# Kernel tuning notes

Hardware: AMD Instinct MI355X
Metric: run time of the kernel (lower is better)

The kernel has to match this reference:

```python
import jax, jax.numpy as jnp
import numpy as np

EMB = 768
BLOCK = 64
K = EMB // BLOCK  # 12


def setup_inputs() -> dict:
    key = jax.random.key(0)
    ks = jax.random.split(key, 8)
    n, c, d, h, E, M, P = 4, 1024, 768, 12, 32, 4, 256
    seq = jax.random.normal(ks[0], (n, c, d), dtype=jnp.float32)
    attn = jax.random.uniform(ks[1], (n, h, c, c), dtype=jnp.float32)
    attn = attn / attn.sum(-1, keepdims=True)  # attention-like rows
    mention_pos = jax.random.randint(ks[2], (n, E, M), 0, c)
    hts = jax.random.randint(ks[3], (n, P, 2), 0, E)
    W_head = jax.random.normal(ks[4], (2 * d, EMB), dtype=jnp.float32) / np.sqrt(2 * d)
    W_tail = jax.random.normal(ks[5], (2 * d, EMB), dtype=jnp.float32) / np.sqrt(2 * d)
    W_bil = jax.random.normal(ks[6], (EMB * BLOCK, 97), dtype=jnp.float32) / np.sqrt(EMB * BLOCK)
    return {
        "sequence_output": seq,
        "attention": attn,
        "mention_pos": mention_pos,
        "hts": hts,
        "W_head": W_head,
        "b_head": jnp.zeros((EMB,), jnp.float32),
        "W_tail": W_tail,
        "b_tail": jnp.zeros((EMB,), jnp.float32),
        "W_bil": W_bil,
        "b_bil": jnp.zeros((97,), jnp.float32),
    }


def reference(sequence_output, attention, mention_pos, hts,
              W_head, b_head, W_tail, b_tail, W_bil, b_bil):
    n, c, d = sequence_output.shape
    h = attention.shape[1]
    P = hts.shape[1]

    bidx = jnp.arange(n)[:, None, None]
    # gather mention token embeddings: [n, E, M, d]
    m_emb = sequence_output[bidx, mention_pos]
    # entity embedding = logsumexp over mentions (single-mention case is identical)
    ent_emb = jax.nn.logsumexp(m_emb, axis=2)                      # [n, E, d]

    # per-mention attention rows: attention[i, :, pos, :] -> [n, E, M, h, c]
    att_t = jnp.transpose(attention, (0, 2, 1, 3))                 # [n, c, h, c]
    m_att = att_t[bidx, mention_pos]                               # [n, E, M, h, c]
    ent_att = m_att.mean(axis=2)                                   # [n, E, h, c]

    pidx = jnp.arange(n)[:, None]
    hs = ent_emb[pidx, hts[..., 0]]                                # [n, P, d]
    ts = ent_emb[pidx, hts[..., 1]]
    h_att = ent_att[pidx, hts[..., 0]]                             # [n, P, h, c]
    t_att = ent_att[pidx, hts[..., 1]]

    ht_att = (h_att * t_att).mean(axis=2)                          # [n, P, c]
    ht_att = ht_att / (ht_att.sum(-1, keepdims=True) + 1e-30)
    # relation context: contract('ld,rl->rd') per doc
    rs = jnp.einsum('ncd,npc->npd', sequence_output, ht_att)       # [n, P, d]

    R = n * P
    hs2 = jnp.tanh(jnp.concatenate([hs, rs], -1).reshape(R, 2 * d) @ W_head + b_head)
    ts2 = jnp.tanh(jnp.concatenate([ts, rs], -1).reshape(R, 2 * d) @ W_tail + b_tail)

    b1 = hs2.reshape(R, K, BLOCK)
    b2 = ts2.reshape(R, K, BLOCK)
    bl = (b1[:, :, :, None] * b2[:, :, None, :]).reshape(R, EMB * BLOCK)
    logits = bl @ W_bil + b_bil                                    # [R, 97]
    return logits
```

## Files before the change

kernel.cpp:

```cpp
#include <hip/hip_runtime.h>
#include <hip/hip_bf16.h>
#include <math.h>

#define ND 4
#define CL 1024
#define DD 768
#define HH 12
#define EE 32
#define MMEN 4
#define PP 256
#define EMBD 768
#define KBL 12
#define OUTD 97
#define RTOT (ND*PP)
#define NSPLIT 48

typedef unsigned short u16;
typedef __attribute__((ext_vector_type(8))) short short8;
typedef __attribute__((ext_vector_type(8))) _Float16 half8;
typedef __attribute__((ext_vector_type(4))) float f32x4;

static __device__ inline float bf16u_to_f(unsigned v){
  union { unsigned u; float f; } c; c.u = v << 16; return c.f;
}
static __device__ inline unsigned f_to_bf16u(float f){
  union { float f; unsigned u; } c; c.f = f;
  return (c.u + 0x7fffu + ((c.u >> 16) & 1u)) >> 16;
}
static __device__ inline u16 f_to_f16u(float f){
  _Float16 h = (_Float16)f;
  union { _Float16 h; u16 u; } c; c.h = h; return c.u;
}

#define GLOAD_LDS16(gp, lp) __builtin_amdgcn_global_load_lds( \
    (const __attribute__((address_space(1))) unsigned*)(gp), \
    (__attribute__((address_space(3))) unsigned*)(lp), 16, 0, 0)

__global__ __launch_bounds__(256) void k_ent_emb(const float* __restrict__ seq,
    const int* __restrict__ mpos, u16* __restrict__ ent_emb_bf,
    float* __restrict__ S)
{
  int idx = blockIdx.x*256 + threadIdx.x;
  if (idx >= ND*EE*DD) return;
  if (idx < RTOT) S[idx] = 0.f;
  int dd = idx % DD;
  int e  = (idx / DD) % EE;
  int i  = idx / (DD*EE);
  const int* mp = mpos + (i*EE + e)*MMEN;
  float v[MMEN];
  float mx = -1e30f;
  #pragma unroll
  for (int m=0;m<MMEN;m++){
    v[m] = seq[(i*CL + mp[m])*DD + dd];
    mx = fmaxf(mx, v[m]);
  }
  float s = 0.f;
  #pragma unroll
  for (int m=0;m<MMEN;m++) s += expf(v[m]-mx);
  ent_emb_bf[idx] = (u16)f_to_bf16u(mx + logf(s));
}

__global__ __launch_bounds__(256) void k_ent_att(const float* __restrict__ attn,
    const int* __restrict__ mpos, u16* __restrict__ ent_att_bf)
{
  int idx = blockIdx.x*256 + threadIdx.x;
  if (idx >= ND*EE*HH*(CL/8)) return;
  int j8   = idx % (CL/8);
  int head = (idx / (CL/8)) % HH;
  int e    = (idx / (CL/8*HH)) % EE;
  int i    = idx / (CL/8*HH*EE);
  const int* mp = mpos + (i*EE + e)*MMEN;
  float acc[8] = {};
  #pragma unroll
  for (int m=0;m<MMEN;m++){
    const float4* p = (const float4*)(attn +
        ((size_t)(i*HH + head)*CL + mp[m])*CL + j8*8);
    float4 a = p[0], b = p[1];
    acc[0]+=a.x; acc[1]+=a.y; acc[2]+=a.z; acc[3]+=a.w;
    acc[4]+=b.x; acc[5]+=b.y; acc[6]+=b.z; acc[7]+=b.w;
  }
  unsigned o[4];
  #pragma unroll
  for (int q=0;q<4;q++){
    unsigned lo = f_to_bf16u(acc[2*q]   * (1.f/MMEN));
    unsigned hi = f_to_bf16u(acc[2*q+1] * (1.f/MMEN));
    o[q] = lo | (hi<<16);
  }
  ((uint4*)ent_att_bf)[idx] = make_uint4(o[0],o[1],o[2],o[3]);
}

__global__ __launch_bounds__(256) void k_ht_att(const u16* __restrict__ ent_att_bf,
    const int* __restrict__ hts, u16* __restrict__ u_ht_bf, float* __restrict__ S)
{
  const int j0  = blockIdx.x*64;
  const int pb  = blockIdx.y*64;
  const int doc = blockIdx.z;
  const int tid = threadIdx.x;
  const int p_local = tid >> 2, quad = tid & 3;
  const int grow = doc*PP + pb + p_local;
  const int he = hts[grow*2+0], te = hts[grow*2+1];
  const u16* ha = ent_att_bf + ((size_t)(doc*EE + he)*HH)*CL;
  const u16* ta = ent_att_bf + ((size_t)(doc*EE + te)*HH)*CL;
  const int jj = j0 + quad*16;

  float acc[16] = {};
  #pragma unroll
  for (int h=0; h<HH; h++){
    const uint4* pa = (const uint4*)(ha + h*CL + jj);
    const uint4* pb4 = (const uint4*)(ta + h*CL + jj);
    uint4 a0 = pa[0], a1 = pa[1];
    uint4 b0 = pb4[0], b1 = pb4[1];
    unsigned ua[8] = {a0.x,a0.y,a0.z,a0.w,a1.x,a1.y,a1.z,a1.w};
    unsigned ub[8] = {b0.x,b0.y,b0.z,b0.w,b1.x,b1.y,b1.z,b1.w};
    #pragma unroll
    for (int q=0;q<8;q++){
      acc[2*q]   += bf16u_to_f(ua[q]&0xffffu) * bf16u_to_f(ub[q]&0xffffu);
      acc[2*q+1] += bf16u_to_f(ua[q]>>16)     * bf16u_to_f(ub[q]>>16);
    }
  }
  float sum = 0.f;
  unsigned o[8];
  #pragma unroll
  for (int q=0;q<8;q++){
    float v0 = acc[2*q]   * (1.f/HH);
    float v1 = acc[2*q+1] * (1.f/HH);
    sum += v0 + v1;
    o[q] = f_to_bf16u(v0) | (f_to_bf16u(v1)<<16);
  }
  uint4* dst = (uint4*)(u_ht_bf + (size_t)grow*CL + jj);
  dst[0] = make_uint4(o[0],o[1],o[2],o[3]);
  dst[1] = make_uint4(o[4],o[5],o[6],o[7]);
  sum += __shfl_xor(sum, 1, 64);
  sum += __shfl_xor(sum, 2, 64);
  if (quad == 0) atomicAdd(&S[grow], sum);
}

__global__ __launch_bounds__(256) void k_transpose_bf(const float* __restrict__ src,
    u16* __restrict__ dst, int R, int C)
{
  size_t boff = (size_t)blockIdx.z * R * C;
  src += boff; dst += boff;
  __shared__ float t[32][33];
  int tx = threadIdx.x & 31, ty = threadIdx.x >> 5;
  int c0 = blockIdx.x*32, r0 = blockIdx.y*32;
  #pragma unroll
  for (int q=0;q<4;q++)
    t[ty+8*q][tx] = src[(size_t)(r0+ty+8*q)*C + c0+tx];
  __syncthreads();
  #pragma unroll
  for (int q=0;q<4;q++)
    dst[(size_t)(c0+ty+8*q)*R + r0+tx] = (u16)f_to_bf16u(t[tx][ty+8*q]);
}

__global__ __launch_bounds__(256) void k_transpose_bf_w(
    const float* __restrict__ srcA, u16* __restrict__ dstA,
    const float* __restrict__ srcB, u16* __restrict__ dstB, int R, int C)
{
  const float* src = blockIdx.z ? srcB : srcA;
  u16* dst         = blockIdx.z ? dstB : dstA;
  __shared__ float t[32][33];
  int tx = threadIdx.x & 31, ty = threadIdx.x >> 5;
  int c0 = blockIdx.x*32, r0 = blockIdx.y*32;
  #pragma unroll
  for (int q=0;q<4;q++)
    t[ty+8*q][tx] = src[(size_t)(r0+ty+8*q)*C + c0+tx];
  __syncthreads();
  #pragma unroll
  for (int q=0;q<4;q++)
    dst[(size_t)(c0+ty+8*q)*R + r0+tx] = (u16)f_to_bf16u(t[tx][ty+8*q]);
}

__global__ __launch_bounds__(256) void k_gemm_rs_mfma(
    const u16* __restrict__ u_ht_bf, const u16* __restrict__ seq_t_bf,
    const float* __restrict__ S, u16* __restrict__ rs_bf)
{
  const int rt = blockIdx.x, ct = blockIdx.y, doc = blockIdx.z;
  const u16* A  = u_ht_bf + (size_t)doc*PP*CL;
  const u16* Bt = seq_t_bf + (size_t)doc*DD*CL;
  const int row0 = rt*128, col0 = ct*64;
  __shared__ __align__(16) u16 As[128*64];
  __shared__ __align__(16) u16 Bs[64*64];
  const int tid = threadIdx.x, lane = tid & 63, wave = tid >> 6;
  const int m = lane & 15, j8 = lane >> 4;
  const int srow8 = lane >> 3, sc8 = lane & 7;
  f32x4 acc[2][4];
  #pragma unroll
  for (int a=0;a<2;a++)
    #pragma unroll
    for (int b=0;b<4;b++) acc[a][b] = (f32x4){0.f,0.f,0.f,0.f};

  for (int k0 = 0; k0 < CL; k0 += 64){
    __syncthreads();
    #pragma unroll
    for (int ii=0; ii<4; ii++){
      int row = ii*32 + wave*8 + srow8;
      int gc = sc8 ^ (row & 7);
      const u16* gp = A + (size_t)(row0+row)*CL + k0 + gc*8;
      GLOAD_LDS16(gp, &As[(ii*32 + wave*8)*64]);
    }
    #pragma unroll
    for (int ii=0; ii<2; ii++){
      int row = ii*32 + wave*8 + srow8;
      int gc = sc8 ^ (row & 7);
      const u16* gp = Bt + (size_t)(col0+row)*CL + k0 + gc*8;
      GLOAD_LDS16(gp, &Bs[(ii*32 + wave*8)*64]);
    }
    __syncthreads();
    #pragma unroll
    for (int h=0; h<2; h++){
      short8 af[2], bf[4];
      #pragma unroll
      for (int mf=0; mf<2; mf++){
        int r = wave*32 + mf*16 + m;
        int c = (h*4 + j8) ^ (r & 7);
        af[mf] = *(const short8*)&As[r*64 + c*8];
      }
      #pragma unroll
      for (int nt=0; nt<4; nt++){
        int n = nt*16 + m;
        int c = (h*4 + j8) ^ (n & 7);
        bf[nt] = *(const short8*)&Bs[n*64 + c*8];
      }
      #pragma unroll
      for (int mf=0; mf<2; mf++)
        #pragma unroll
        for (int nt=0; nt<4; nt++)
          acc[mf][nt] = __builtin_amdgcn_mfma_f32_16x16x32_bf16(af[mf], bf[nt], acc[mf][nt], 0,0,0);
    }
  }

  #pragma unroll
  for (int mf=0; mf<2; mf++){
    #pragma unroll
    for (int nt=0; nt<4; nt++){
      int colg = col0 + nt*16 + m;
      #pragma unroll
      for (int reg=0; reg<4; reg++){
        int rowg = doc*PP + row0 + wave*32 + mf*16 + j8*4 + reg;
        float sc = 1.f / (S[rowg] + 1e-30f);
        rs_bf[(size_t)rowg*DD + colg] = (u16)f_to_bf16u(acc[mf][nt][reg] * sc);
      }
    }
  }
}

__global__ __launch_bounds__(256) void k_gemm_ht_mfma(
    const u16* __restrict__ ent_emb_bf, const u16* __restrict__ rs_bf,
    const int* __restrict__ hts,
    const u16* __restrict__ Wht, const u16* __restrict__ Wtt,
    const float* __restrict__ b_head, const float* __restrict__ b_tail,
    u16* __restrict__ hs2h, u16* __restrict__ ts2h)
{
  const int rt = blockIdx.x, ct = blockIdx.y, z = blockIdx.z;
  const u16* Bt   = z ? Wtt : Wht;
  const float* bias = z ? b_tail : b_head;
  u16* C          = z ? ts2h : hs2h;
  const int row0 = rt*128, col0 = ct*64;
  __shared__ __align__(16) u16 As[128*64];
  __shared__ __align__(16) u16 Bs[64*64];
  const int tid = threadIdx.x, lane = tid & 63, wave = tid >> 6;
  const int m = lane & 15, j8 = lane >> 4;
  const int srow8 = lane >> 3, sc8 = lane & 7;

  const u16* gEnt[4]; const u16* gRs[4]; int gcA[4];
  #pragma unroll
  for (int ii=0; ii<4; ii++){
    int row  = ii*32 + wave*8 + srow8;
    int grow = row0 + row;
    int ent  = hts[grow*2 + z];
    gEnt[ii] = ent_emb_bf + ((size_t)((grow>>8)*EE + ent))*DD;
    gRs[ii]  = rs_bf + (size_t)grow*DD;
    gcA[ii]  = (sc8 ^ (row & 7)) * 8;
  }

  f32x4 acc[2][4];
  #pragma unroll
  for (int a=0;a<2;a++)
    #pragma unroll
    for (int b=0;b<4;b++) acc[a][b] = (f32x4){0.f,0.f,0.f,0.f};

  for (int k0 = 0; k0 < 1536; k0 += 64){
    __syncthreads();
    #pragma unroll
    for (int ii=0; ii<4; ii++){
      const u16* gp = (k0 < DD) ? (gEnt[ii] + k0 + gcA[ii])
                                : (gRs[ii] + (k0-DD) + gcA[ii]);
      GLOAD_LDS16(gp, &As[(ii*32 + wave*8)*64]);
    }
    #pragma unroll
    for (int ii=0; ii<2; ii++){
      int row = ii*32 + wave*8 + srow8;
      int gc = sc8 ^ (row & 7);
      const u16* gp = Bt + (size_t)(col0+row)*1536 + k0 + gc*8;
      GLOAD_LDS16(gp, &Bs[(ii*32 + wave*8)*64]);
    }
    __syncthreads();
    #pragma unroll
    for (int h=0; h<2; h++){
      short8 af[2], bf[4];
      #pragma unroll
      for (int mf=0; mf<2; mf++){
        int r = wave*32 + mf*16 + m;
        int c = (h*4 + j8) ^ (r & 7);
        af[mf] = *(const short8*)&As[r*64 + c*8];
      }
      #pragma unroll
      for (int nt=0; nt<4; nt++){
        int n = nt*16 + m;
        int c = (h*4 + j8) ^ (n & 7);
        bf[nt] = *(const short8*)&Bs[n*64 + c*8];
      }
      #pragma unroll
      for (int mf=0; mf<2; mf++)
        #pragma unroll
        for (int nt=0; nt<4; nt++)
          acc[mf][nt] = __builtin_amdgcn_mfma_f32_16x16x32_bf16(af[mf], bf[nt], acc[mf][nt], 0,0,0);
    }
  }

  #pragma unroll
  for (int mf=0; mf<2; mf++){
    #pragma unroll
    for (int nt=0; nt<4; nt++){
      int colg = col0 + nt*16 + m;
      float bv = bias[colg];
      #pragma unroll
      for (int reg=0; reg<4; reg++){
        int rowg = row0 + wave*32 + mf*16 + j8*4 + reg;
        C[(size_t)rowg*DD + colg] = f_to_f16u(tanhf(acc[mf][nt][reg] + bv));
      }
    }
  }
}

__global__ __launch_bounds__(256) void k_wt2(const float* __restrict__ W_bil,
    u16* __restrict__ Wt2)
{
  const int cc = blockIdx.x;
  __shared__ u16 lds2[4480];
  int tid = threadIdx.x;
  for (int u=tid; u<4480; u+=256) lds2[u] = 0;
  __syncthreads();
  for (int u=tid; u<112*32; u+=256){
    int kk = u / 112, n = u % 112;
    if (n < OUTD)
      lds2[n*40 + kk] = f_to_f16u(W_bil[(size_t)(cc*32 + kk)*OUTD + n]);
  }
  __syncthreads();
  uint4* dst = (uint4*)(Wt2 + (size_t)cc*4480);
  const uint4* src = (const uint4*)lds2;
  for (int v=tid; v<560; v+=256) dst[v] = src[v];
}

__global__ __launch_bounds__(256) void k_bilinear(
    const u16* __restrict__ hs2h, const u16* __restrict__ ts2h,
    const u16* __restrict__ Wt2, float* __restrict__ pbuf)
{
  const int rt = blockIdx.x;
  const int sp = blockIdx.y;
  const int kb = sp >> 2;
  const int i0 = (sp & 3) * 16;
  const int row0 = rt * 128;

  __shared__ __align__(16) u16 b1s[128][24];
  __shared__ __align__(16) u16 b2s[128][72];
  __shared__ __align__(16) u16 Ws[4480];

  const int tid = threadIdx.x;
  const int lane = tid & 63, wave = tid >> 6;
  const int m = lane & 15, j8 = lane >> 4;

  {
    int r = tid >> 1, half = tid & 1;
    uint4 v = *(const uint4*)&hs2h[(size_t)(row0+r)*EMBD + kb*64 + i0 + half*8];
    *(uint4*)&b1s[r][half*8] = v;
  }
  for (int u=tid; u<1024; u+=256){
    int r = u >> 3, seg = u & 7;
    uint4 v = *(const uint4*)&ts2h[(size_t)(row0+r)*EMBD + kb*64 + seg*8];
    *(uint4*)&b2s[r][seg*8] = v;
  }

  const uint4* gsrc = (const uint4*)(Wt2 + (size_t)(sp*32)*4480);
  uint4* ws4 = (uint4*)Ws;
  uint4 pf0, pf1, pf2;
  {
    pf0 = gsrc[tid];
    pf1 = gsrc[tid+256];
    if (tid < 48) pf2 = gsrc[tid+512];
  }

  f32x4 acc[2][7];
  #pragma unroll
  for (int f=0;f<2;f++)
    #pragma unroll
    for (int nt=0;nt<7;nt++) acc[f][nt] = (f32x4){0.f,0.f,0.f,0.f};

  for (int c=0; c<32; c++){
    __syncthreads();
    ws4[tid] = pf0; ws4[tid+256] = pf1; if (tid < 48) ws4[tid+512] = pf2;
    if (c+1 < 32){
      size_t b = (size_t)(c+1)*560;
      pf0 = gsrc[b+tid];
      pf1 = gsrc[b+tid+256];
      if (tid < 48) pf2 = gsrc[b+tid+512];
    }
    __syncthreads();

    const int i_rel = c >> 1;
    const int j0 = (c & 1) * 32;

    half8 bfr[7];
    #pragma unroll
    for (int nt=0;nt<7;nt++)
      bfr[nt] = *(const half8*)&Ws[(nt*16 + m)*40 + j8*8];

    #pragma unroll
    for (int f=0;f<2;f++){
      int r = wave*32 + f*16 + m;
      _Float16 s = *(const _Float16*)&b1s[r][i_rel];
      half8 sv = {s,s,s,s,s,s,s,s};
      half8 b2v = *(const half8*)&b2s[r][j0 + j8*8];
      half8 af = sv * b2v;
      #pragma unroll
      for (int nt=0;nt<7;nt++)
        acc[f][nt] = __builtin_amdgcn_mfma_f32_16x16x32_f16(af, bfr[nt], acc[f][nt], 0, 0, 0);
    }
  }

  float* dst = pbuf + ((size_t)sp*RTOT + row0)*112;
  #pragma unroll
  for (int f=0;f<2;f++){
    #pragma unroll
    for (int nt=0;nt<7;nt++){
      int col = nt*16 + m;
      #pragma unroll
      for (int reg=0;reg<4;reg++){
        int lrow = wave*32 + f*16 + j8*4 + reg;
        dst[(size_t)lrow*112 + col] = acc[f][nt][reg];
      }
    }
  }
}

__global__ __launch_bounds__(256) void k_reduce_logits(
    const float* __restrict__ pbuf, const float* __restrict__ b_bil,
    float* __restrict__ logits)
{
  int idx = blockIdx.x*256 + threadIdx.x;
  if (idx >= RTOT*112) return;
  int col = idx % 112, row = idx / 112;
  if (col >= OUTD) return;
  float s0 = 0.f, s1 = 0.f, s2 = 0.f, s3 = 0.f;
  const size_t stride = (size_t)RTOT*112;
  #pragma unroll
  for (int sp=0; sp<NSPLIT; sp+=4){
    s0 += pbuf[(sp+0)*stride + idx];
    s1 += pbuf[(sp+1)*stride + idx];
    s2 += pbuf[(sp+2)*stride + idx];
    s3 += pbuf[(sp+3)*stride + idx];
  }
  logits[(size_t)row*OUTD + col] = (s0+s1) + (s2+s3) + b_bil[col];
}

extern "C" void kernel_launch(void* const* d_in, const int* in_sizes, int n_in,
                              void* d_out, int out_size, void* d_ws, size_t ws_size,
                              hipStream_t stream)
{
  const float* seq    = (const float*)d_in[0];
  const float* attn   = (const float*)d_in[1];
  const int*   mpos   = (const int*)d_in[2];
  const int*   hts    = (const int*)d_in[3];
  const float* W_head = (const float*)d_in[4];
  const float* b_head = (const float*)d_in[5];
  const float* W_tail = (const float*)d_in[6];
  const float* b_tail = (const float*)d_in[7];
  const float* W_bil  = (const float*)d_in[8];
  const float* b_bil  = (const float*)d_in[9];
  float* logits = (float*)d_out;

  float* ws = (float*)d_ws;
  u16*   ent_emb_bf = (u16*)(ws + 0);
  float* S          = ws + 49152;
  u16*   rs_bf      = (u16*)(ws + 50176);
  u16*   hs2h       = (u16*)(ws + 443392);
  u16*   ts2h       = (u16*)(ws + 836608);
  u16*   Wh_t       = (u16*)(ws + 1229824);
  u16*   Wt_t       = (u16*)(ws + 1819648);
  u16*   ent_att_bf = (u16*)(ws + 2409472);
  u16*   u_ht_bf    = (u16*)(ws + 3195904);
  u16*   seq_t_bf   = (u16*)(ws + 3720192);
  u16*   Wt2        = (u16*)(ws + 5293056);
  float* pbuf       = ws + 8733696;

  k_ent_emb<<<(ND*EE*DD+255)/256, 256, 0, stream>>>(seq, mpos, ent_emb_bf, S);
  k_ent_att<<<(ND*EE*HH*(CL/8)+255)/256, 256, 0, stream>>>(attn, mpos, ent_att_bf);
  k_ht_att<<<dim3(16, 4, 4), 256, 0, stream>>>(ent_att_bf, hts, u_ht_bf, S);
  k_transpose_bf<<<dim3(DD/32, CL/32, ND), 256, 0, stream>>>(seq, seq_t_bf, CL, DD);
  k_transpose_bf_w<<<dim3(DD/32, 1536/32, 2), 256, 0, stream>>>(
      W_head, Wh_t, W_tail, Wt_t, 1536, DD);
  k_gemm_rs_mfma<<<dim3(2, 12, 4), 256, 0, stream>>>(u_ht_bf, seq_t_bf, S, rs_bf);
  k_gemm_ht_mfma<<<dim3(8, 12, 2), 256, 0, stream>>>(ent_emb_bf, rs_bf, hts,
      Wh_t, Wt_t, b_head, b_tail, hs2h, ts2h);
  k_wt2<<<1536, 256, 0, stream>>>(W_bil, Wt2);
  k_bilinear<<<dim3(RTOT/128, NSPLIT), 256, 0, stream>>>(hs2h, ts2h, Wt2, pbuf);
  k_reduce_logits<<<(RTOT*112+255)/256, 256, 0, stream>>>(pbuf, b_bil, logits);
}
```

Before: 359.7 us.

## Merge preprocessing kernels into one launch and halve rs GEMM row tile

Five independent preprocessing kernels (entity embedding, entity attention, sequence transpose, weight transposes, W_bil repack) are combined into one kernel that dispatches on block index. This cuts launch count and lets the small phases share the GPU at the same time. The rs GEMM also moves from a 128-row to a 64-row tile, doubling its grid from 96 to 192 blocks for better CU occupancy, at the cost of reloading more B tiles. The merged kernel reserves both LDS buffers for every block, which may lower occupancy.

```diff
diff --git a/kernel.cpp b/kernel.cpp
--- a/kernel.cpp
+++ b/kernel.cpp
@@ -36,57 +36,114 @@
     (const __attribute__((address_space(1))) unsigned*)(gp), \
     (__attribute__((address_space(3))) unsigned*)(lp), 16, 0, 0)
 
-__global__ __launch_bounds__(256) void k_ent_emb(const float* __restrict__ seq,
-    const int* __restrict__ mpos, u16* __restrict__ ent_emb_bf,
-    float* __restrict__ S)
-{
-  int idx = blockIdx.x*256 + threadIdx.x;
-  if (idx >= ND*EE*DD) return;
-  if (idx < RTOT) S[idx] = 0.f;
-  int dd = idx % DD;
-  int e  = (idx / DD) % EE;
-  int i  = idx / (DD*EE);
-  const int* mp = mpos + (i*EE + e)*MMEN;
-  float v[MMEN];
-  float mx = -1e30f;
-  #pragma unroll
-  for (int m=0;m<MMEN;m++){
-    v[m] = seq[(i*CL + mp[m])*DD + dd];
-    mx = fmaxf(mx, v[m]);
-  }
-  float s = 0.f;
-  #pragma unroll
-  for (int m=0;m<MMEN;m++) s += expf(v[m]-mx);
-  ent_emb_bf[idx] = (u16)f_to_bf16u(mx + logf(s));
-}
-
-__global__ __launch_bounds__(256) void k_ent_att(const float* __restrict__ attn,
-    const int* __restrict__ mpos, u16* __restrict__ ent_att_bf)
-{
-  int idx = blockIdx.x*256 + threadIdx.x;
-  if (idx >= ND*EE*HH*(CL/8)) return;
-  int j8   = idx % (CL/8);
-  int head = (idx / (CL/8)) % HH;
-  int e    = (idx / (CL/8*HH)) % EE;
-  int i    = idx / (CL/8*HH*EE);
-  const int* mp = mpos + (i*EE + e)*MMEN;
-  float acc[8] = {};
-  #pragma unroll
-  for (int m=0;m<MMEN;m++){
-    const float4* p = (const float4*)(attn +
-        ((size_t)(i*HH + head)*CL + mp[m])*CL + j8*8);
-    float4 a = p[0], b = p[1];
-    acc[0]+=a.x; acc[1]+=a.y; acc[2]+=a.z; acc[3]+=a.w;
-    acc[4]+=b.x; acc[5]+=b.y; acc[6]+=b.z; acc[7]+=b.w;
-  }
-  unsigned o[4];
-  #pragma unroll
-  for (int q=0;q<4;q++){
-    unsigned lo = f_to_bf16u(acc[2*q]   * (1.f/MMEN));
-    unsigned hi = f_to_bf16u(acc[2*q+1] * (1.f/MMEN));
-    o[q] = lo | (hi<<16);
-  }
-  ((uint4*)ent_att_bf)[idx] = make_uint4(o[0],o[1],o[2],o[3]);
+__global__ __launch_bounds__(256) void k_preproc(
+    const float* __restrict__ seq, const float* __restrict__ attn,
+    const int* __restrict__ mpos,
+    const float* __restrict__ W_head, const float* __restrict__ W_tail,
+    const float* __restrict__ W_bil,
+    u16* __restrict__ ent_emb_bf, u16* __restrict__ ent_att_bf,
+    u16* __restrict__ seq_t_bf, u16* __restrict__ Wh_t, u16* __restrict__ Wt_t,
+    u16* __restrict__ Wt2, float* __restrict__ S)
+{
+  __shared__ float t[32][33];
+  __shared__ __align__(16) u16 lds2[4480];
+  const int bid = blockIdx.x;
+  const int tid = threadIdx.x;
+
+  if (bid < 384) {
+    int idx = bid*256 + tid;
+    if (idx < RTOT) S[idx] = 0.f;
+    int dd = idx % DD;
+    int e  = (idx / DD) % EE;
+    int i  = idx / (DD*EE);
+    const int* mp = mpos + (i*EE + e)*MMEN;
+    float v[MMEN];
+    float mx = -1e30f;
+    #pragma unroll
+    for (int m=0;m<MMEN;m++){
+      v[m] = seq[(i*CL + mp[m])*DD + dd];
+      mx = fmaxf(mx, v[m]);
+    }
+    float s = 0.f;
+    #pragma unroll
+    for (int m=0;m<MMEN;m++) s += expf(v[m]-mx);
+    ent_emb_bf[idx] = (u16)f_to_bf16u(mx + logf(s));
+  }
+  else if (bid < 1152) {
+    int idx = (bid-384)*256 + tid;
+    int j8   = idx % (CL/8);
+    int head = (idx / (CL/8)) % HH;
+    int e    = (idx / (CL/8*HH)) % EE;
+    int i    = idx / (CL/8*HH*EE);
+    const int* mp = mpos + (i*EE + e)*MMEN;
+    float acc[8] = {};
+    #pragma unroll
+    for (int m=0;m<MMEN;m++){
+      const float4* p = (const float4*)(attn +
+          ((size_t)(i*HH + head)*CL + mp[m])*CL + j8*8);
+      float4 a = p[0], b = p[1];
+      acc[0]+=a.x; acc[1]+=a.y; acc[2]+=a.z; acc[3]+=a.w;
+      acc[4]+=b.x; acc[5]+=b.y; acc[6]+=b.z; acc[7]+=b.w;
+    }
+    unsigned o[4];
+    #pragma unroll
+    for (int q=0;q<4;q++){
+      unsigned lo = f_to_bf16u(acc[2*q]   * (1.f/MMEN));
+      unsigned hi = f_to_bf16u(acc[2*q+1] * (1.f/MMEN));
+      o[q] = lo | (hi<<16);
+    }
+    ((uint4*)ent_att_bf)[idx] = make_uint4(o[0],o[1],o[2],o[3]);
+  }
+  else if (bid < 4224) {
+    int l = bid - 1152;
+    int bx = l % 24;
+    int by = (l / 24) % 32;
+    int bz = l / 768;
+    const int R = CL, C = DD;
+    const float* src = seq + (size_t)bz*R*C;
+    u16* dst = seq_t_bf + (size_t)bz*R*C;
+    int tx = tid & 31, ty = tid >> 5;
+    int c0 = bx*32, r0 = by*32;
+    #pragma unroll
+    for (int q=0;q<4;q++)
+      t[ty+8*q][tx] = src[(size_t)(r0+ty+8*q)*C + c0+tx];
+    __syncthreads();
+    #pragma unroll
+    for (int q=0;q<4;q++)
+      dst[(size_t)(c0+ty+8*q)*R + r0+tx] = (u16)f_to_bf16u(t[tx][ty+8*q]);
+  }
+  else if (bid < 6528) {
+    int l = bid - 4224;
+    int bx = l % 24;
+    int by = (l / 24) % 48;
+    int bz = l / 1152;
+    const int R = 1536, C = DD;
+    const float* src = bz ? W_tail : W_head;
+    u16* dst         = bz ? Wt_t   : Wh_t;
+    int tx = tid & 31, ty = tid >> 5;
+    int c0 = bx*32, r0 = by*32;
+    #pragma unroll
+    for (int q=0;q<4;q++)
+      t[ty+8*q][tx] = src[(size_t)(r0+ty+8*q)*C + c0+tx];
+    __syncthreads();
+    #pragma unroll
+    for (int q=0;q<4;q++)
+      dst[(size_t)(c0+ty+8*q)*R + r0+tx] = (u16)f_to_bf16u(t[tx][ty+8*q]);
+  }
+  else {
+    int cc = bid - 6528;
+    for (int u=tid; u<4480; u+=256) lds2[u] = 0;
+    __syncthreads();
+    for (int u=tid; u<112*32; u+=256){
+      int kk = u / 112, n = u % 112;
+      if (n < OUTD)
+        lds2[n*40 + kk] = f_to_f16u(W_bil[(size_t)(cc*32 + kk)*OUTD + n]);
+    }
+    __syncthreads();
+    uint4* dst = (uint4*)(Wt2 + (size_t)cc*4480);
+    const uint4* src = (const uint4*)lds2;
+    for (int v=tid; v<560; v+=256) dst[v] = src[v];
+  }
 }
 
 __global__ __launch_bounds__(256) void k_ht_att(const u16* __restrict__ ent_att_bf,
@@ -135,41 +192,6 @@
   if (quad == 0) atomicAdd(&S[grow], sum);
 }
 
-__global__ __launch_bounds__(256) void k_transpose_bf(const float* __restrict__ src,
-    u16* __restrict__ dst, int R, int C)
-{
-  size_t boff = (size_t)blockIdx.z * R * C;
-  src += boff; dst += boff;
-  __shared__ float t[32][33];
-  int tx = threadIdx.x & 31, ty = threadIdx.x >> 5;
-  int c0 = blockIdx.x*32, r0 = blockIdx.y*32;
-  #pragma unroll
-  for (int q=0;q<4;q++)
-    t[ty+8*q][tx] = src[(size_t)(r0+ty+8*q)*C + c0+tx];
-  __syncthreads();
-  #pragma unroll
-  for (int q=0;q<4;q++)
-    dst[(size_t)(c0+ty+8*q)*R + r0+tx] = (u16)f_to_bf16u(t[tx][ty+8*q]);
-}
-
-__global__ __launch_bounds__(256) void k_transpose_bf_w(
-    const float* __restrict__ srcA, u16* __restrict__ dstA,
-    const float* __restrict__ srcB, u16* __restrict__ dstB, int R, int C)
-{
-  const float* src = blockIdx.z ? srcB : srcA;
-  u16* dst         = blockIdx.z ? dstB : dstA;
-  __shared__ float t[32][33];
-  int tx = threadIdx.x & 31, ty = threadIdx.x >> 5;
-  int c0 = blockIdx.x*32, r0 = blockIdx.y*32;
-  #pragma unroll
-  for (int q=0;q<4;q++)
-    t[ty+8*q][tx] = src[(size_t)(r0+ty+8*q)*C + c0+tx];
-  __syncthreads();
-  #pragma unroll
-  for (int q=0;q<4;q++)
-    dst[(size_t)(c0+ty+8*q)*R + r0+tx] = (u16)f_to_bf16u(t[tx][ty+8*q]);
-}
-
 __global__ __launch_bounds__(256) void k_gemm_rs_mfma(
     const u16* __restrict__ u_ht_bf, const u16* __restrict__ seq_t_bf,
     const float* __restrict__ S, u16* __restrict__ rs_bf)
@@ -177,43 +199,35 @@
   const int rt = blockIdx.x, ct = blockIdx.y, doc = blockIdx.z;
   const u16* A  = u_ht_bf + (size_t)doc*PP*CL;
   const u16* Bt = seq_t_bf + (size_t)doc*DD*CL;
-  const int row0 = rt*128, col0 = ct*64;
-  __shared__ __align__(16) u16 As[128*64];
+  const int row0 = rt*64, col0 = ct*64;
+  __shared__ __align__(16) u16 As[64*64];
   __shared__ __align__(16) u16 Bs[64*64];
   const int tid = threadIdx.x, lane = tid & 63, wave = tid >> 6;
   const int m = lane & 15, j8 = lane >> 4;
   const int srow8 = lane >> 3, sc8 = lane & 7;
-  f32x4 acc[2][4];
-  #pragma unroll
-  for (int a=0;a<2;a++)
-    #pragma unroll
-    for (int b=0;b<4;b++) acc[a][b] = (f32x4){0.f,0.f,0.f,0.f};
+  f32x4 acc[4];
+  #pragma unroll
+  for (int b=0;b<4;b++) acc[b] = (f32x4){0.f,0.f,0.f,0.f};
 
   for (int k0 = 0; k0 < CL; k0 += 64){
     __syncthreads();
-    #pragma unroll
-    for (int ii=0; ii<4; ii++){
-      int row = ii*32 + wave*8 + srow8;
-      int gc = sc8 ^ (row & 7);
-      const u16* gp = A + (size_t)(row0+row)*CL + k0 + gc*8;
-      GLOAD_LDS16(gp, &As[(ii*32 + wave*8)*64]);
-    }
     #pragma unroll
     for (int ii=0; ii<2; ii++){
       int row = ii*32 + wave*8 + srow8;
       int gc = sc8 ^ (row & 7);
-      const u16* gp = Bt + (size_t)(col0+row)*CL + k0 + gc*8;
-      GLOAD_LDS16(gp, &Bs[(ii*32 + wave*8)*64]);
+      const u16* gpA = A + (size_t)(row0+row)*CL + k0 + gc*8;
+      GLOAD_LDS16(gpA, &As[(ii*32 + wave*8)*64]);
+      const u16* gpB = Bt + (size_t)(col0+row)*CL + k0 + gc*8;
+      GLOAD_LDS16(gpB, &Bs[(ii*32 + wave*8)*64]);
     }
     __syncthreads();
     #pragma unroll
     for (int h=0; h<2; h++){
-      short8 af[2], bf[4];
-      #pragma unroll
-      for (int mf=0; mf<2; mf++){
-        int r = wave*32 + mf*16 + m;
+      short8 af, bf[4];
+      {
+        int r = wave*16 + m;
         int c = (h*4 + j8) ^ (r & 7);
-        af[mf] = *(const short8*)&As[r*64 + c*8];
+        af = *(const short8*)&As[r*64 + c*8];
       }
       #pragma unroll
       for (int nt=0; nt<4; nt++){
@@ -222,24 +236,19 @@
         bf[nt] = *(const short8*)&Bs[n*64 + c*8];
       }
       #pragma unroll
-      for (int mf=0; mf<2; mf++)
-        #pragma unroll
-        for (int nt=0; nt<4; nt++)
-          acc[mf][nt] = __builtin_amdgcn_mfma_f32_16x16x32_bf16(af[mf], bf[nt], acc[mf][nt], 0,0,0);
-    }
-  }
-
-  #pragma unroll
-  for (int mf=0; mf<2; mf++){
-    #pragma unroll
-    for (int nt=0; nt<4; nt++){
-      int colg = col0 + nt*16 + m;
-      #pragma unroll
-      for (int reg=0; reg<4; reg++){
-        int rowg = doc*PP + row0 + wave*32 + mf*16 + j8*4 + reg;
-        float sc = 1.f / (S[rowg] + 1e-30f);
-        rs_bf[(size_t)rowg*DD + colg] = (u16)f_to_bf16u(acc[mf][nt][reg] * sc);
-      }
+      for (int nt=0; nt<4; nt++)
+        acc[nt] = __builtin_amdgcn_mfma_f32_16x16x32_bf16(af, bf[nt], acc[nt], 0,0,0);
+    }
+  }
+
+  #pragma unroll
+  for (int nt=0; nt<4; nt++){
+    int colg = col0 + nt*16 + m;
+    #pragma unroll
+    for (int reg=0; reg<4; reg++){
+      int rowg = doc*PP + row0 + wave*16 + j8*4 + reg;
+      float sc = 1.f / (S[rowg] + 1e-30f);
+      rs_bf[(size_t)rowg*DD + colg] = (u16)f_to_bf16u(acc[nt][reg] * sc);
     }
   }
 }
@@ -331,25 +340,6 @@
       }
     }
   }
-}
-
-__global__ __launch_bounds__(256) void k_wt2(const float* __restrict__ W_bil,
-    u16* __restrict__ Wt2)
-{
-  const int cc = blockIdx.x;
-  __shared__ u16 lds2[4480];
-  int tid = threadIdx.x;
-  for (int u=tid; u<4480; u+=256) lds2[u] = 0;
-  __syncthreads();
-  for (int u=tid; u<112*32; u+=256){
-    int kk = u / 112, n = u % 112;
-    if (n < OUTD)
-      lds2[n*40 + kk] = f_to_f16u(W_bil[(size_t)(cc*32 + kk)*OUTD + n]);
-  }
-  __syncthreads();
-  uint4* dst = (uint4*)(Wt2 + (size_t)cc*4480);
-  const uint4* src = (const uint4*)lds2;
-  for (int v=tid; v<560; v+=256) dst[v] = src[v];
 }
 
 __global__ __launch_bounds__(256) void k_bilinear(
@@ -493,16 +483,12 @@
   u16*   Wt2        = (u16*)(ws + 5293056);
   float* pbuf       = ws + 8733696;
 
-  k_ent_emb<<<(ND*EE*DD+255)/256, 256, 0, stream>>>(seq, mpos, ent_emb_bf, S);
-  k_ent_att<<<(ND*EE*HH*(CL/8)+255)/256, 256, 0, stream>>>(attn, mpos, ent_att_bf);
+  k_preproc<<<8064, 256, 0, stream>>>(seq, attn, mpos, W_head, W_tail, W_bil,
+      ent_emb_bf, ent_att_bf, seq_t_bf, Wh_t, Wt_t, Wt2, S);
   k_ht_att<<<dim3(16, 4, 4), 256, 0, stream>>>(ent_att_bf, hts, u_ht_bf, S);
-  k_transpose_bf<<<dim3(DD/32, CL/32, ND), 256, 0, stream>>>(seq, seq_t_bf, CL, DD);
-  k_transpose_bf_w<<<dim3(DD/32, 1536/32, 2), 256, 0, stream>>>(
-      W_head, Wh_t, W_tail, Wt_t, 1536, DD);
-  k_gemm_rs_mfma<<<dim3(2, 12, 4), 256, 0, stream>>>(u_ht_bf, seq_t_bf, S, rs_bf);
+  k_gemm_rs_mfma<<<dim3(4, 12, 4), 256, 0, stream>>>(u_ht_bf, seq_t_bf, S, rs_bf);
   k_gemm_ht_mfma<<<dim3(8, 12, 2), 256, 0, stream>>>(ent_emb_bf, rs_bf, hts,
       Wh_t, Wt_t, b_head, b_tail, hs2h, ts2h);
-  k_wt2<<<1536, 256, 0, stream>>>(W_bil, Wt2);
   k_bilinear<<<dim3(RTOT/128, NSPLIT), 256, 0, stream>>>(hs2h, ts2h, Wt2, pbuf);
   k_reduce_logits<<<(RTOT*112+255)/256, 256, 0, stream>>>(pbuf, b_bil, logits);
 }
```

New measurement: 346.3 us. -3.7%, faster.
